# Kernel optimization log

Hardware: AMD Instinct MI355X
Metric: run time of the kernel (lower is better)

The kernel has to match this reference:

```python
import jax, jax.numpy as jnp
import numpy as np

B, T, D, H, O, E, K = 2, 2048, 1024, 4096, 1024, 8, 2


def setup_inputs() -> dict:
    key = jax.random.key(0)
    ks = jax.random.split(key, 10)
    s = 0.02  # small init scale to keep activations well-conditioned
    return {
        "x": jax.random.normal(ks[0], (B, T, D), jnp.float32),
        "noise": jax.random.normal(ks[1], (B, T, E), jnp.float32),
        "Wg": jax.random.normal(ks[2], (D, E), jnp.float32) * s,
        "bg": jnp.zeros((E,), jnp.float32),
        "Wn": jax.random.normal(ks[3], (D, E), jnp.float32) * s,
        "bn": jnp.zeros((E,), jnp.float32),
        "W1": jax.random.normal(ks[4], (E, D, H), jnp.float32) * s,
        "b1": jnp.zeros((E, H), jnp.float32),
        "W2": jax.random.normal(ks[5], (E, H, O), jnp.float32) * s,
        "b2": jnp.zeros((E, O), jnp.float32),
    }


def reference(x, noise, Wg, bg, Wn, bn, W1, b1, W2, b2):
    # --- NoisyTopkRouter ---
    logits = x @ Wg + bg                    # [B,T,E]
    noise_logits = x @ Wn + bn              # [B,T,E]
    noisy = logits + noise * jax.nn.softplus(noise_logits)
    top_v, top_i = jax.lax.top_k(noisy, K)  # [B,T,K]
    # scatter top-k logits into a -inf background, softmax -> sparse gates
    mask = jax.nn.one_hot(top_i, E, dtype=noisy.dtype).sum(-2)  # [B,T,E] in {0,1}
    sparse_logits = jnp.where(mask > 0, noisy, -jnp.inf)
    gating = jax.nn.softmax(sparse_logits, axis=-1)
    # mask + L1 normalize (F.normalize p=1, dim=2)
    gating = gating * mask
    gating = gating / jnp.maximum(jnp.sum(jnp.abs(gating), axis=-1, keepdims=True), 1e-12)
    # --- dense run of ALL experts (faithful to the naive torch module) ---
    h = jax.nn.relu(jnp.einsum('btd,edh->beth', x, W1) + b1[:, None, :])   # [B,E,T,H]
    expert_out = jnp.einsum('beth,eho->beto', h, W2) + b2[:, None, :]       # [B,E,T,O]
    # combine: torch transposes to [B,T,E,O] then einsum 'bte,bteo->bto'
    out = jnp.einsum('bte,beto->bto', gating, expert_out)                   # [B,T,O]
    return out
```

## Files before the change

### kernel.cpp

```cpp
#include <hip/hip_runtime.h>
#include <hip/hip_bf16.h>

#define TOK 4096
#define DD  1024
#define HH  4096
#define OO  1024
#define EE  8
#define MAX_SLOTS 80

typedef float  f32x4  __attribute__((ext_vector_type(4)));
typedef __bf16 bf16x8 __attribute__((ext_vector_type(8)));
typedef __bf16 bf16x4 __attribute__((ext_vector_type(4)));
typedef unsigned int u32x4 __attribute__((ext_vector_type(4)));

union ABCast { u32x4 u; bf16x8 b; };

__global__ void router_kernel(const float* __restrict__ x, const float* __restrict__ noise,
                              const float* __restrict__ Wg, const float* __restrict__ bg,
                              const float* __restrict__ Wn, const float* __restrict__ bn,
                              int* __restrict__ topk_e, float* __restrict__ topk_g,
                              int* __restrict__ cnt)
{
    int wave = threadIdx.x >> 6;
    int lane = threadIdx.x & 63;
    int token = blockIdx.x * 4 + wave;
    const float* xr = x + (size_t)token * DD;
    float accg[EE], accn[EE];
#pragma unroll
    for (int e = 0; e < EE; ++e) { accg[e] = 0.f; accn[e] = 0.f; }
    for (int jj = 0; jj < DD / 64; ++jj) {
        int d = lane + jj * 64;
        float xv = xr[d];
        const float* wgr = Wg + d * EE;
        const float* wnr = Wn + d * EE;
#pragma unroll
        for (int e = 0; e < EE; ++e) {
            accg[e] += xv * wgr[e];
            accn[e] += xv * wnr[e];
        }
    }
#pragma unroll
    for (int off = 32; off; off >>= 1) {
#pragma unroll
        for (int e = 0; e < EE; ++e) {
            accg[e] += __shfl_down(accg[e], off, 64);
            accn[e] += __shfl_down(accn[e], off, 64);
        }
    }
    if (lane == 0) {
        float noisy[EE];
#pragma unroll
        for (int e = 0; e < EE; ++e) {
            float lg = accg[e] + bg[e];
            float nl = accn[e] + bn[e];
            float sp = fmaxf(nl, 0.f) + log1pf(expf(-fabsf(nl)));
            noisy[e] = lg + noise[(size_t)token * EE + e] * sp;
        }
        int i1 = 0; float v1 = noisy[0];
#pragma unroll
        for (int e = 1; e < EE; ++e) if (noisy[e] > v1) { v1 = noisy[e]; i1 = e; }
        int i2 = -1; float v2 = -1e30f;
#pragma unroll
        for (int e = 0; e < EE; ++e) if (e != i1 && noisy[e] > v2) { v2 = noisy[e]; i2 = e; }
        float ex = expf(v2 - v1);
        float g1 = 1.f / (1.f + ex);
        float g2 = ex / (1.f + ex);
        topk_e[token * 2] = i1;  topk_e[token * 2 + 1] = i2;
        topk_g[token * 2] = g1;  topk_g[token * 2 + 1] = g2;
        atomicAdd(&cnt[i1], 1);
        atomicAdd(&cnt[i2], 1);
    }
}

__global__ void plan_kernel(const int* __restrict__ cnt, int* __restrict__ base_row,
                            int* __restrict__ slot_e, int* __restrict__ slot_m,
                            int* __restrict__ fill)
{
    if (threadIdx.x == 0 && blockIdx.x == 0) {
        int s = 0;
        for (int e = 0; e < EE; ++e) {
            base_row[e] = s * 128;
            int tiles = (cnt[e] + 127) >> 7;
            for (int t = 0; t < tiles; ++t) { slot_e[s] = e; slot_m[s] = t; ++s; }
            fill[e] = 0;
        }
        for (int s2 = s; s2 < MAX_SLOTS; ++s2) { slot_e[s2] = -1; slot_m[s2] = 0; }
    }
}

__global__ void scatter_kernel(const int* __restrict__ topk_e, const float* __restrict__ topk_g,
                               const int* __restrict__ base_row, int* __restrict__ fill,
                               int* __restrict__ row_token, float* __restrict__ row_gate)
{
    int t = blockIdx.x * blockDim.x + threadIdx.x;
    if (t >= TOK * 2) return;
    int e = topk_e[t];
    int pos = atomicAdd(&fill[e], 1);
    int row = base_row[e] + pos;
    row_token[row] = t >> 1;
    row_gate[row] = topk_g[t];
}

__global__ void convert_x_kernel(const float* __restrict__ in, __bf16* __restrict__ out)
{
    int i = blockIdx.x * blockDim.x + threadIdx.x;
    f32x4 v = ((const f32x4*)in)[i];
    bf16x4 o;
    o.x = (__bf16)v.x; o.y = (__bf16)v.y; o.z = (__bf16)v.z; o.w = (__bf16)v.w;
    ((bf16x4*)out)[i] = o;
}

__global__ void transpose_cvt_kernel(const float* __restrict__ in, __bf16* __restrict__ out,
                                     int R, int C)
{
    __shared__ __bf16 tile[32][33];
    int e = blockIdx.z;
    const float* ine = in + (size_t)e * R * C;
    __bf16* oute = out + (size_t)e * R * C;
    int tx = threadIdx.x & 31, ty = threadIdx.x >> 5;
    int c0 = blockIdx.x * 32, r0 = blockIdx.y * 32;
#pragma unroll
    for (int i = 0; i < 4; ++i) {
        int r = r0 + ty + i * 8;
        tile[ty + i * 8][tx] = (__bf16)ine[(size_t)r * C + c0 + tx];
    }
    __syncthreads();
#pragma unroll
    for (int i = 0; i < 4; ++i) {
        int c = c0 + ty + i * 8;
        oute[(size_t)c * R + r0 + tx] = tile[tx][ty + i * 8];
    }
}

__global__ void gemm1_kernel(const __bf16* __restrict__ xb,
                             const __bf16* __restrict__ W1t,
                             const float* __restrict__ b1bias,
                             const int* __restrict__ slot_e, const int* __restrict__ slot_m,
                             const int* __restrict__ base_row, const int* __restrict__ cnt,
                             const int* __restrict__ row_token,
                             __bf16* __restrict__ h)
{
    int slot = blockIdx.y;
    int e = slot_e[slot];
    if (e < 0) return;
    int mt = slot_m[slot];
    int row0 = base_row[e] + mt * 128;
    int rows_in = min(128, cnt[e] - mt * 128);
    int n0 = blockIdx.x * 128;

    __shared__ u32x4 Alds[4 * 128];
    __shared__ u32x4 Blds[4 * 128];

    int tid = threadIdx.x;
    int rs = tid >> 2;
    int kc = tid & 3;
    int rA0 = rs, rA1 = rs + 64;
    int tok0 = (rA0 < rows_in) ? row_token[row0 + rA0] : 0;
    int tok1 = (rA1 < rows_in) ? row_token[row0 + rA1] : 0;
    const __bf16* aptr0 = xb + (size_t)tok0 * DD + kc * 8;
    const __bf16* aptr1 = xb + (size_t)tok1 * DD + kc * 8;
    const __bf16* bbase = W1t + (size_t)e * HH * DD + (size_t)n0 * DD + kc * 8;
    const __bf16* bptr0 = bbase + (size_t)rA0 * DD;
    const __bf16* bptr1 = bbase + (size_t)rA1 * DD;

    int wave = tid >> 6, lane = tid & 63;
    int wm = wave & 1, wn = wave >> 1;
    int quad = lane >> 4, l16 = lane & 15;

    f32x4 acc[4][4];
#pragma unroll
    for (int i = 0; i < 4; ++i)
#pragma unroll
        for (int j = 0; j < 4; ++j) acc[i][j] = (f32x4)(0.0f);

    for (int k0 = 0; k0 < DD; k0 += 32) {
        u32x4 a0 = *(const u32x4*)(aptr0 + k0);
        u32x4 a1 = *(const u32x4*)(aptr1 + k0);
        u32x4 bld0 = *(const u32x4*)(bptr0 + k0);
        u32x4 bld1 = *(const u32x4*)(bptr1 + k0);
        __syncthreads();
        Alds[kc * 128 + rA0] = a0;
        Alds[kc * 128 + rA1] = a1;
        Blds[kc * 128 + rA0] = bld0;
        Blds[kc * 128 + rA1] = bld1;
        __syncthreads();
        ABCast af[4], bfr[4];
#pragma unroll
        for (int mf = 0; mf < 4; ++mf) af[mf].u = Alds[quad * 128 + wm * 64 + mf * 16 + l16];
#pragma unroll
        for (int nf = 0; nf < 4; ++nf) bfr[nf].u = Blds[quad * 128 + wn * 64 + nf * 16 + l16];
#pragma unroll
        for (int mf = 0; mf < 4; ++mf)
#pragma unroll
            for (int nf = 0; nf < 4; ++nf)
                acc[mf][nf] = __builtin_amdgcn_mfma_f32_16x16x32_bf16(af[mf].b, bfr[nf].b, acc[mf][nf], 0, 0, 0);
    }

#pragma unroll
    for (int mf = 0; mf < 4; ++mf) {
        int rl = wm * 64 + mf * 16 + quad * 4;
#pragma unroll
        for (int i = 0; i < 4; ++i) {
            int rli = rl + i;
            if (rli < rows_in) {
                size_t hrow = (size_t)(row0 + rli) * HH;
#pragma unroll
                for (int nf = 0; nf < 4; ++nf) {
                    int col = n0 + wn * 64 + nf * 16 + l16;
                    float v = acc[mf][nf][i] + b1bias[e * HH + col];
                    v = fmaxf(v, 0.f);
                    h[hrow + col] = (__bf16)v;
                }
            }
        }
    }
}

__global__ void gemm2_kernel(const __bf16* __restrict__ h,
                             const __bf16* __restrict__ W2t,
                             const float* __restrict__ b2bias,
                             const int* __restrict__ slot_e, const int* __restrict__ slot_m,
                             const int* __restrict__ base_row, const int* __restrict__ cnt,
                             const int* __restrict__ row_token, const float* __restrict__ row_gate,
                             float* __restrict__ out)
{
    int slot = blockIdx.y;
    int e = slot_e[slot];
    if (e < 0) return;
    int mt = slot_m[slot];
    int row0 = base_row[e] + mt * 128;
    int rows_in = min(128, cnt[e] - mt * 128);
    int n0 = blockIdx.x * 128;

    __shared__ u32x4 Alds[4 * 128];
    __shared__ u32x4 Blds[4 * 128];

    int tid = threadIdx.x;
    int rs = tid >> 2;
    int kc = tid & 3;
    int rA0 = rs, rA1 = rs + 64;
    const __bf16* abase = h + (size_t)row0 * HH + kc * 8;
    const __bf16* aptr0 = abase + (size_t)rA0 * HH;
    const __bf16* aptr1 = abase + (size_t)rA1 * HH;
    const __bf16* bbase = W2t + (size_t)e * OO * HH + (size_t)n0 * HH + kc * 8;
    const __bf16* bptr0 = bbase + (size_t)rA0 * HH;
    const __bf16* bptr1 = bbase + (size_t)rA1 * HH;

    int wave = tid >> 6, lane = tid & 63;
    int wm = wave & 1, wn = wave >> 1;
    int quad = lane >> 4, l16 = lane & 15;

    f32x4 acc[4][4];
#pragma unroll
    for (int i = 0; i < 4; ++i)
#pragma unroll
        for (int j = 0; j < 4; ++j) acc[i][j] = (f32x4)(0.0f);

    for (int k0 = 0; k0 < HH; k0 += 32) {
        u32x4 a0 = *(const u32x4*)(aptr0 + k0);
        u32x4 a1 = *(const u32x4*)(aptr1 + k0);
        u32x4 bld0 = *(const u32x4*)(bptr0 + k0);
        u32x4 bld1 = *(const u32x4*)(bptr1 + k0);
        __syncthreads();
        Alds[kc * 128 + rA0] = a0;
        Alds[kc * 128 + rA1] = a1;
        Blds[kc * 128 + rA0] = bld0;
        Blds[kc * 128 + rA1] = bld1;
        __syncthreads();
        ABCast af[4], bfr[4];
#pragma unroll
        for (int mf = 0; mf < 4; ++mf) af[mf].u = Alds[quad * 128 + wm * 64 + mf * 16 + l16];
#pragma unroll
        for (int nf = 0; nf < 4; ++nf) bfr[nf].u = Blds[quad * 128 + wn * 64 + nf * 16 + l16];
#pragma unroll
        for (int mf = 0; mf < 4; ++mf)
#pragma unroll
            for (int nf = 0; nf < 4; ++nf)
                acc[mf][nf] = __builtin_amdgcn_mfma_f32_16x16x32_bf16(af[mf].b, bfr[nf].b, acc[mf][nf], 0, 0, 0);
    }

#pragma unroll
    for (int mf = 0; mf < 4; ++mf) {
        int rl = wm * 64 + mf * 16 + quad * 4;
#pragma unroll
        for (int i = 0; i < 4; ++i) {
            int rli = rl + i;
            if (rli < rows_in) {
                int token = row_token[row0 + rli];
                float gate = row_gate[row0 + rli];
                float* orow = out + (size_t)token * OO;
#pragma unroll
                for (int nf = 0; nf < 4; ++nf) {
                    int col = n0 + wn * 64 + nf * 16 + l16;
                    float v = acc[mf][nf][i] + b2bias[e * OO + col];
                    atomicAdd(&orow[col], gate * v);
                }
            }
        }
    }
}

extern "C" void kernel_launch(void* const* d_in, const int* in_sizes, int n_in,
                              void* d_out, int out_size, void* d_ws, size_t ws_size,
                              hipStream_t stream)
{
    const float* x     = (const float*)d_in[0];
    const float* noise = (const float*)d_in[1];
    const float* Wg    = (const float*)d_in[2];
    const float* bg    = (const float*)d_in[3];
    const float* Wn    = (const float*)d_in[4];
    const float* bn    = (const float*)d_in[5];
    const float* W1    = (const float*)d_in[6];
    const float* b1    = (const float*)d_in[7];
    const float* W2    = (const float*)d_in[8];
    const float* b2    = (const float*)d_in[9];
    float* out = (float*)d_out;

    char* p = (char*)d_ws;
    auto alloc = [&](size_t bytes) { char* r = p; p += (bytes + 255) & ~(size_t)255; return r; };
    __bf16* xb   = (__bf16*)alloc((size_t)TOK * DD * 2);
    __bf16* W1t  = (__bf16*)alloc((size_t)EE * DD * HH * 2);
    __bf16* W2t  = (__bf16*)alloc((size_t)EE * HH * OO * 2);
    __bf16* hbuf = (__bf16*)alloc((size_t)MAX_SLOTS * 128 * HH * 2);
    int*   topk_e    = (int*)alloc((size_t)TOK * 2 * 4);
    float* topk_g    = (float*)alloc((size_t)TOK * 2 * 4);
    int*   row_token = (int*)alloc((size_t)MAX_SLOTS * 128 * 4);
    float* row_gate  = (float*)alloc((size_t)MAX_SLOTS * 128 * 4);
    int*   cnt       = (int*)alloc(EE * 4);
    int*   fill      = (int*)alloc(EE * 4);
    int*   base_row  = (int*)alloc(EE * 4);
    int*   slot_e    = (int*)alloc(MAX_SLOTS * 4);
    int*   slot_m    = (int*)alloc(MAX_SLOTS * 4);

    hipMemsetAsync(out, 0, (size_t)out_size * 4, stream);
    hipMemsetAsync(cnt, 0, EE * 4, stream);

    router_kernel<<<TOK / 4, 256, 0, stream>>>(x, noise, Wg, bg, Wn, bn, topk_e, topk_g, cnt);
    plan_kernel<<<1, 64, 0, stream>>>(cnt, base_row, slot_e, slot_m, fill);
    scatter_kernel<<<(TOK * 2) / 256, 256, 0, stream>>>(topk_e, topk_g, base_row, fill, row_token, row_gate);
    convert_x_kernel<<<(TOK * DD / 4) / 256, 256, 0, stream>>>(x, xb);
    transpose_cvt_kernel<<<dim3(HH / 32, DD / 32, EE), 256, 0, stream>>>(W1, W1t, DD, HH);
    transpose_cvt_kernel<<<dim3(OO / 32, HH / 32, EE), 256, 0, stream>>>(W2, W2t, HH, OO);
    gemm1_kernel<<<dim3(HH / 128, MAX_SLOTS), 256, 0, stream>>>(xb, W1t, b1, slot_e, slot_m,
                                                                base_row, cnt, row_token, hbuf);
    gemm2_kernel<<<dim3(OO / 128, MAX_SLOTS), 256, 0, stream>>>(hbuf, W2t, b2, slot_e, slot_m,
                                                                base_row, cnt, row_token, row_gate, out);
}
```

Measured before the change: 784.0 us.

## Load GEMM tiles directly into LDS and split GEMM2 K across two blocks

Both expert GEMMs now fill their shared-memory tiles with global_load_lds instructions, which write straight into LDS instead of staging through VGPRs and issuing separate ds_write stores. GEMM2 gains a split-K grid dimension of 2 so each block covers half of H. This doubles the number of blocks on a grid that only has 8 column tiles, and the partial sums are combined through the existing atomic adds, with the bias applied only by the first split. The cost is twice as many atomic adds into the output. Row-major A rows beyond rows_in in GEMM2 still read h rows past the expert's range, as before.

```diff
diff --git a/kernel.cpp b/kernel.cpp
--- a/kernel.cpp
+++ b/kernel.cpp
@@ -14,6 +14,13 @@
 typedef unsigned int u32x4 __attribute__((ext_vector_type(4)));
 
 union ABCast { u32x4 u; bf16x8 b; };
+
+typedef __attribute__((address_space(3))) unsigned int       lds_uint;
+typedef const __attribute__((address_space(1))) unsigned int glob_uint;
+
+__device__ __forceinline__ void gload_lds16(void* lds, const void* g) {
+    __builtin_amdgcn_global_load_lds((glob_uint*)g, (lds_uint*)lds, 16, 0, 0);
+}
 
 __global__ void router_kernel(const float* __restrict__ x, const float* __restrict__ noise,
                               const float* __restrict__ Wg, const float* __restrict__ bg,
@@ -148,23 +155,22 @@
     int rows_in = min(128, cnt[e] - mt * 128);
     int n0 = blockIdx.x * 128;
 
-    __shared__ u32x4 Alds[4 * 128];
-    __shared__ u32x4 Blds[4 * 128];
+    __shared__ u32x4 Alds[512];
+    __shared__ u32x4 Blds[512];
 
     int tid = threadIdx.x;
-    int rs = tid >> 2;
-    int kc = tid & 3;
-    int rA0 = rs, rA1 = rs + 64;
-    int tok0 = (rA0 < rows_in) ? row_token[row0 + rA0] : 0;
-    int tok1 = (rA1 < rows_in) ? row_token[row0 + rA1] : 0;
-    const __bf16* aptr0 = xb + (size_t)tok0 * DD + kc * 8;
-    const __bf16* aptr1 = xb + (size_t)tok1 * DD + kc * 8;
-    const __bf16* bbase = W1t + (size_t)e * HH * DD + (size_t)n0 * DD + kc * 8;
-    const __bf16* bptr0 = bbase + (size_t)rA0 * DD;
-    const __bf16* bptr1 = bbase + (size_t)rA1 * DD;
-
-    int wave = tid >> 6, lane = tid & 63;
-    int wm = wave & 1, wn = wave >> 1;
+    int wv = tid >> 6, lane = tid & 63;
+
+    int ar0 = tid & 127,        ak0 = tid >> 7;
+    int ar1 = ar0,              ak1 = ak0 + 2;
+    int tok0 = (ar0 < rows_in) ? row_token[row0 + ar0] : 0;
+    const char* ag0 = (const char*)(xb + (size_t)tok0 * DD + ak0 * 8);
+    const char* ag1 = (const char*)(xb + (size_t)tok0 * DD + ak1 * 8);
+    const __bf16* bbase = W1t + (size_t)e * HH * DD + (size_t)n0 * DD;
+    const char* bg0 = (const char*)(bbase + (size_t)ar0 * DD + ak0 * 8);
+    const char* bg1 = (const char*)(bbase + (size_t)ar1 * DD + ak1 * 8);
+
+    int wm = wv & 1, wn = wv >> 1;
     int quad = lane >> 4, l16 = lane & 15;
 
     f32x4 acc[4][4];
@@ -173,16 +179,12 @@
 #pragma unroll
         for (int j = 0; j < 4; ++j) acc[i][j] = (f32x4)(0.0f);
 
-    for (int k0 = 0; k0 < DD; k0 += 32) {
-        u32x4 a0 = *(const u32x4*)(aptr0 + k0);
-        u32x4 a1 = *(const u32x4*)(aptr1 + k0);
-        u32x4 bld0 = *(const u32x4*)(bptr0 + k0);
-        u32x4 bld1 = *(const u32x4*)(bptr1 + k0);
+    for (int kb = 0; kb < DD * 2; kb += 64) {
         __syncthreads();
-        Alds[kc * 128 + rA0] = a0;
-        Alds[kc * 128 + rA1] = a1;
-        Blds[kc * 128 + rA0] = bld0;
-        Blds[kc * 128 + rA1] = bld1;
+        gload_lds16(&Alds[wv * 64],       ag0 + kb);
+        gload_lds16(&Alds[256 + wv * 64], ag1 + kb);
+        gload_lds16(&Blds[wv * 64],       bg0 + kb);
+        gload_lds16(&Blds[256 + wv * 64], bg1 + kb);
         __syncthreads();
         ABCast af[4], bfr[4];
 #pragma unroll
@@ -231,23 +233,23 @@
     int row0 = base_row[e] + mt * 128;
     int rows_in = min(128, cnt[e] - mt * 128);
     int n0 = blockIdx.x * 128;
-
-    __shared__ u32x4 Alds[4 * 128];
-    __shared__ u32x4 Blds[4 * 128];
+    int kz = blockIdx.z;
+
+    __shared__ u32x4 Alds[512];
+    __shared__ u32x4 Blds[512];
 
     int tid = threadIdx.x;
-    int rs = tid >> 2;
-    int kc = tid & 3;
-    int rA0 = rs, rA1 = rs + 64;
-    const __bf16* abase = h + (size_t)row0 * HH + kc * 8;
-    const __bf16* aptr0 = abase + (size_t)rA0 * HH;
-    const __bf16* aptr1 = abase + (size_t)rA1 * HH;
-    const __bf16* bbase = W2t + (size_t)e * OO * HH + (size_t)n0 * HH + kc * 8;
-    const __bf16* bptr0 = bbase + (size_t)rA0 * HH;
-    const __bf16* bptr1 = bbase + (size_t)rA1 * HH;
-
-    int wave = tid >> 6, lane = tid & 63;
-    int wm = wave & 1, wn = wave >> 1;
+    int wv = tid >> 6, lane = tid & 63;
+
+    int ar0 = tid & 127, ak0 = tid >> 7;
+    int ak1 = ak0 + 2;
+    const char* ag0 = (const char*)(h + (size_t)(row0 + ar0) * HH + ak0 * 8);
+    const char* ag1 = (const char*)(h + (size_t)(row0 + ar0) * HH + ak1 * 8);
+    const __bf16* bbase = W2t + (size_t)e * OO * HH + (size_t)n0 * HH;
+    const char* bg0 = (const char*)(bbase + (size_t)ar0 * HH + ak0 * 8);
+    const char* bg1 = (const char*)(bbase + (size_t)ar0 * HH + ak1 * 8);
+
+    int wm = wv & 1, wn = wv >> 1;
     int quad = lane >> 4, l16 = lane & 15;
 
     f32x4 acc[4][4];
@@ -256,16 +258,13 @@
 #pragma unroll
         for (int j = 0; j < 4; ++j) acc[i][j] = (f32x4)(0.0f);
 
-    for (int k0 = 0; k0 < HH; k0 += 32) {
-        u32x4 a0 = *(const u32x4*)(aptr0 + k0);
-        u32x4 a1 = *(const u32x4*)(aptr1 + k0);
-        u32x4 bld0 = *(const u32x4*)(bptr0 + k0);
-        u32x4 bld1 = *(const u32x4*)(bptr1 + k0);
+    int kb0 = kz * 4096;
+    for (int kb = kb0; kb < kb0 + 4096; kb += 64) {
         __syncthreads();
-        Alds[kc * 128 + rA0] = a0;
-        Alds[kc * 128 + rA1] = a1;
-        Blds[kc * 128 + rA0] = bld0;
-        Blds[kc * 128 + rA1] = bld1;
+        gload_lds16(&Alds[wv * 64],       ag0 + kb);
+        gload_lds16(&Alds[256 + wv * 64], ag1 + kb);
+        gload_lds16(&Blds[wv * 64],       bg0 + kb);
+        gload_lds16(&Blds[256 + wv * 64], bg1 + kb);
         __syncthreads();
         ABCast af[4], bfr[4];
 #pragma unroll
@@ -292,7 +291,8 @@
 #pragma unroll
                 for (int nf = 0; nf < 4; ++nf) {
                     int col = n0 + wn * 64 + nf * 16 + l16;
-                    float v = acc[mf][nf][i] + b2bias[e * OO + col];
+                    float v = acc[mf][nf][i];
+                    if (kz == 0) v += b2bias[e * OO + col];
                     atomicAdd(&orow[col], gate * v);
                 }
             }
@@ -343,6 +343,6 @@
     transpose_cvt_kernel<<<dim3(OO / 32, HH / 32, EE), 256, 0, stream>>>(W2, W2t, HH, OO);
     gemm1_kernel<<<dim3(HH / 128, MAX_SLOTS), 256, 0, stream>>>(xb, W1t, b1, slot_e, slot_m,
                                                                 base_row, cnt, row_token, hbuf);
-    gemm2_kernel<<<dim3(OO / 128, MAX_SLOTS), 256, 0, stream>>>(hbuf, W2t, b2, slot_e, slot_m,
-                                                                base_row, cnt, row_token, row_gate, out);
-}
+    gemm2_kernel<<<dim3(OO / 128, MAX_SLOTS, 2), 256, 0, stream>>>(hbuf, W2t, b2, slot_e, slot_m,
+                                                                   base_row, cnt, row_token, row_gate, out);
+}
```

After: 902.8 us. 1.15x slower.
